# Optimization experiments

Hardware: AMD Instinct MI355X
Metric: run time of the kernel (lower is better)

## Reference

```python
import jax, jax.numpy as jnp
import numpy as np

D, S, E, MPE = 256, 128, 512, 4096
B, N = 2, 4096


def _rope(x):
    # x: (..., n, d); RoPE over axis -2 positions (dim=1 in the torch code)
    n, d = x.shape[-2], x.shape[-1]
    half = d // 2
    pos = jnp.arange(n, dtype=x.dtype)
    inv_freq = 10000.0 ** (-jnp.arange(half, dtype=x.dtype) / half)
    sinusoid = pos[:, None] * inv_freq  # (n, half)
    sin, cos = jnp.sin(sinusoid), jnp.cos(sinusoid)
    x1, x2 = jnp.split(x, 2, axis=-1)
    return jnp.concatenate([x1 * cos - x2 * sin, x2 * cos + x1 * sin], axis=-1)


def setup_inputs() -> dict:
    key = jax.random.key(0)
    ks = jax.random.split(key, 12)
    std = 0.02
    return {
        "query": jax.random.normal(ks[0], (B, N, D), jnp.float32),
        "ln_w": jnp.ones((D,), jnp.float32),
        "ln_b": jnp.zeros((D,), jnp.float32),
        "Wu": jax.random.normal(ks[1], (D, E), jnp.float32) / np.float32(np.sqrt(D)),
        "bu": jnp.zeros((E,), jnp.float32),
        "Wv": jax.random.normal(ks[2], (D, E), jnp.float32) / np.float32(np.sqrt(D)),
        "bv": jnp.zeros((E,), jnp.float32),
        "Wbase": jax.random.normal(ks[3], (D, S), jnp.float32) / np.float32(np.sqrt(D)),
        "bbase": jnp.zeros((S,), jnp.float32),
        "q_w": jax.random.normal(ks[4], (1, S), jnp.float32) * std,
        "q_b": jnp.zeros((1, S), jnp.float32),
        "k_w": jax.random.normal(ks[5], (1, S), jnp.float32) * std,
        "k_b": jnp.zeros((1, S), jnp.float32),
        "w_rel": jax.random.normal(ks[6], (2 * MPE - 1,), jnp.float32) * std,
        "Wo": jax.random.normal(ks[7], (E, D), jnp.float32) / np.float32(np.sqrt(E)),
        "bo": jnp.zeros((D,), jnp.float32),
    }


def reference(query, ln_w, ln_b, Wu, bu, Wv, bv, Wbase, bbase,
              q_w, q_b, k_w, k_b, w_rel, Wo, bo):
    mpe = (w_rel.shape[0] + 1) // 2
    bsz, n, d = query.shape
    # LayerNorm
    mu = query.mean(axis=-1, keepdims=True)
    var = ((query - mu) ** 2).mean(axis=-1, keepdims=True)
    x = (query - mu) * jax.lax.rsqrt(var + 1e-5) * ln_w + ln_b
    # gated projections
    u = jax.nn.silu(x @ Wu + bu)       # (B,N,E)
    v = jax.nn.silu(x @ Wv + bv)       # (B,N,E)
    base = jax.nn.silu(x @ Wbase + bbase)  # (B,N,S)
    q = _rope(base * q_w + q_b)
    k = _rope(base * k_w + k_b)
    qk = jnp.einsum('bms,bns->bmn', q, k)  # (B,N,N)
    # Toeplitz relative-position bias: bias[i,j] = w_rel[mpe-1 + j - i]
    # (equivalent to the torch pad/repeat/reshape construction, sliced to n)
    i = jnp.arange(n)
    bias = w_rel[(mpe - 1) + i[None, :] - i[:, None]]  # (N,N)
    kernel = jnp.square(jax.nn.relu(qk / mpe + bias))
    out = (u * jnp.einsum('bmn,bne->bme', kernel, v)) @ Wo + bo
    return out
```

## Files before the change

kernel.cpp:

```cpp
#include <hip/hip_runtime.h>
#include <hip/hip_bf16.h>
#include <math.h>

typedef __bf16 bf16_8 __attribute__((ext_vector_type(8)));
typedef float f32x4 __attribute__((ext_vector_type(4)));

#define D_ 256
#define S_ 128
#define E_ 512
#define MPE_ 4096
#define B_ 2
#define N_ 4096
#define M_TOT (B_*N_)

__device__ __forceinline__ ushort f2b(float f) {
  union { float f; uint u; } x; x.f = f;
  uint r = (x.u + 0x7FFFu + ((x.u >> 16) & 1u)) >> 16;
  return (ushort)r;
}
__device__ __forceinline__ float b2f(ushort b) {
  union { uint u; float f; } x; x.u = ((uint)b) << 16;
  return x.f;
}

__device__ __forceinline__ void gl_lds16(const void* g, void* l) {
  __builtin_amdgcn_global_load_lds(
      (const __attribute__((address_space(1))) void*)g,
      (__attribute__((address_space(3))) void*)l, 16, 0, 0);
}

__global__ __launch_bounds__(256) void ln_kernel(const float* __restrict__ q,
    const float* __restrict__ w, const float* __restrict__ b,
    ushort* __restrict__ x) {
  int wid = threadIdx.x >> 6, lane = threadIdx.x & 63;
  int row = blockIdx.x * 4 + wid;
  const float* qr = q + (size_t)row * D_;
  float4 v = *(const float4*)(qr + lane * 4);
  float s  = v.x + v.y + v.z + v.w;
  float ss = v.x*v.x + v.y*v.y + v.z*v.z + v.w*v.w;
  #pragma unroll
  for (int off = 32; off; off >>= 1) {
    s  += __shfl_xor(s, off);
    ss += __shfl_xor(ss, off);
  }
  float mu   = s * (1.0f / 256.0f);
  float var  = ss * (1.0f / 256.0f) - mu * mu;
  float rstd = rsqrtf(var + 1e-5f);
  ushort4 o;
  float vv[4] = {v.x, v.y, v.z, v.w};
  ushort ot[4];
  #pragma unroll
  for (int j = 0; j < 4; ++j) {
    int c = lane * 4 + j;
    ot[j] = f2b((vv[j] - mu) * rstd * w[c] + b[c]);
  }
  o.x = ot[0]; o.y = ot[1]; o.z = ot[2]; o.w = ot[3];
  *(ushort4*)(x + (size_t)row * D_ + lane * 4) = o;
}

__global__ void wt_kernel(const float* __restrict__ in, ushort* __restrict__ out,
                          int R, int C) {
  int o = blockIdx.x * 256 + threadIdx.x;
  if (o >= R * C) return;
  int c = o / R, r = o - c * R;
  out[o] = f2b(in[r * C + c]);
}

template<int EPI>
__global__ __launch_bounds__(256) void gemm_kernel(
    const ushort* __restrict__ A, const ushort* __restrict__ Bt,
    const float* __restrict__ bias, void* __restrict__ out,
    int M, int N, int K) {
  __shared__ alignas(16) ushort As[128 * 64];
  __shared__ alignas(16) ushort Bs[64 * 64];
  int tid = threadIdx.x;
  int lane = tid & 63, wid = tid >> 6;
  int m0 = blockIdx.x * 128, n0 = blockIdx.y * 64;
  int r16 = lane & 15, kq = lane >> 4;
  f32x4 acc[2][4] = {};
  for (int k0 = 0; k0 < K; k0 += 64) {
    __syncthreads();
    #pragma unroll
    for (int t = 0; t < 4; ++t) {
      int cid = tid + t * 256;
      int row = cid >> 3, c = cid & 7;
      uint4 d = *(const uint4*)(A + ((size_t)(m0 + row) * K + k0 + c * 8));
      *(uint4*)&As[row * 64 + ((c ^ (row & 7)) * 8)] = d;
    }
    #pragma unroll
    for (int t = 0; t < 2; ++t) {
      int cid = tid + t * 256;
      int row = cid >> 3, c = cid & 7;
      uint4 d = *(const uint4*)(Bt + ((size_t)(n0 + row) * K + k0 + c * 8));
      *(uint4*)&Bs[row * 64 + ((c ^ (row & 7)) * 8)] = d;
    }
    __syncthreads();
    #pragma unroll
    for (int ks = 0; ks < 2; ++ks) {
      bf16_8 af[2], bfr[4];
      int c = ks * 4 + kq;
      #pragma unroll
      for (int fm = 0; fm < 2; ++fm) {
        int r = wid * 32 + fm * 16 + r16;
        af[fm] = *(const bf16_8*)&As[r * 64 + ((c ^ (r & 7)) * 8)];
      }
      #pragma unroll
      for (int fn = 0; fn < 4; ++fn) {
        int r = fn * 16 + r16;
        bfr[fn] = *(const bf16_8*)&Bs[r * 64 + ((c ^ (r & 7)) * 8)];
      }
      #pragma unroll
      for (int fm = 0; fm < 2; ++fm)
        #pragma unroll
        for (int fn = 0; fn < 4; ++fn)
          acc[fm][fn] = __builtin_amdgcn_mfma_f32_16x16x32_bf16(af[fm], bfr[fn], acc[fm][fn], 0, 0, 0);
    }
  }
  #pragma unroll
  for (int fm = 0; fm < 2; ++fm)
    #pragma unroll
    for (int fn = 0; fn < 4; ++fn)
      #pragma unroll
      for (int reg = 0; reg < 4; ++reg) {
        int ml = wid * 32 + fm * 16 + kq * 4 + reg;
        int nl = fn * 16 + r16;
        size_t gm = m0 + ml, gn = n0 + nl;
        float val = acc[fm][fn][reg] + bias[gn];
        if (EPI == 0) {
          float y = val / (1.0f + expf(-val));
          ((ushort*)out)[gm * N + gn] = f2b(y);
        } else if (EPI == 2) {
          float y = val / (1.0f + expf(-val));
          ((ushort*)out)[gn * (size_t)M_TOT + gm] = f2b(y);
        } else {
          ((float*)out)[gm * N + gn] = val;
        }
      }
}

__global__ __launch_bounds__(256) void rope_kernel(const ushort* __restrict__ base,
    const float* __restrict__ qw, const float* __restrict__ qb,
    const float* __restrict__ kw, const float* __restrict__ kb,
    ushort* __restrict__ Q, ushort* __restrict__ Kk) {
  int g = blockIdx.x * 256 + threadIdx.x;
  int row = g >> 6, i = g & 63;
  int n = row & (N_ - 1);
  float invf = powf(10000.0f, -(float)i * (1.0f / 64.0f));
  float sv, cv;
  sincosf((float)n * invf, &sv, &cv);
  const float sc = 0.015625f;
  float b1 = b2f(base[row * S_ + i]), b2 = b2f(base[row * S_ + 64 + i]);
  float x1q = b1 * qw[i] + qb[i], x2q = b2 * qw[64 + i] + qb[64 + i];
  Q[row * S_ + i]      = f2b((x1q * cv - x2q * sv) * sc);
  Q[row * S_ + 64 + i] = f2b((x2q * cv + x1q * sv) * sc);
  float x1k = b1 * kw[i] + kb[i], x2k = b2 * kw[64 + i] + kb[64 + i];
  Kk[row * S_ + i]      = f2b((x1k * cv - x2k * sv) * sc);
  Kk[row * S_ + 64 + i] = f2b((x2k * cv + x1k * sv) * sc);
}

__global__ __launch_bounds__(512, 2) void attn_kernel(
    const ushort* __restrict__ Q, const ushort* __restrict__ Kd,
    const ushort* __restrict__ VT, const ushort* __restrict__ U,
    const float* __restrict__ w_rel, ushort* __restrict__ KVU) {
  __shared__ alignas(16) ushort Ks[2][64 * 128];
  __shared__ alignas(16) ushort Vs[2][128 * 64];
  __shared__ alignas(16) ushort Pb[128 * 64];
  __shared__ alignas(16) float WrLc[2][4][200];
  const int tid = threadIdx.x, lane = tid & 63, wid = tid >> 6;
  const int b = blockIdx.z, m0 = blockIdx.x * 128, e0 = blockIdx.y * 128;
  const int r16 = lane & 15, kq = lane >> 4;
  const int wqm = wid >> 2, wqn = wid & 3;
  const int wpm = wid >> 1, wpe = wid & 1;

  bf16_8 qf[4][4];
  #pragma unroll
  for (int fm = 0; fm < 4; ++fm)
    #pragma unroll
    for (int ks = 0; ks < 4; ++ks)
      qf[fm][ks] = *(const bf16_8*)(Q +
          ((size_t)(b * N_ + m0 + wqm * 64 + fm * 16 + r16) * S_ + ks * 32 + kq * 8));

  auto stage_kv = [&](int bi, int t) {
    int n0s = t * 64;
    #pragma unroll
    for (int tt = 0; tt < 2; ++tt) {
      int p = tt * 512 + tid;
      int row = p >> 4, sc2 = p & 15;
      int cc = sc2 ^ (row & 7);
      gl_lds16(Kd + ((size_t)(b * N_ + n0s + row) * S_ + cc * 8),
               &Ks[bi][(tt * 512 + wid * 64) * 8]);
    }
    #pragma unroll
    for (int tt = 0; tt < 2; ++tt) {
      int p = tt * 512 + tid;
      int er = p >> 3, sc2 = p & 7;
      int nc = sc2 ^ (er & 7);
      gl_lds16(VT + ((size_t)(e0 + er) * M_TOT + b * N_ + n0s + nc * 8),
               &Vs[bi][(tt * 512 + wid * 64) * 8]);
    }
  };

  const int bi0 = tid, bi1 = tid + 512;
  const int bc0 = bi0 / 200, bx0 = bi0 - bc0 * 200;
  const int bc1 = bi1 / 200, bx1 = bi1 - bc1 * 200;
  const bool bp1 = bi1 < 800;
  auto wr_load = [&](int t, float& w0, float& w1) {
    int W0 = 3968 + t * 64 - m0;
    int i0 = W0 + bx0 - 1 - bc0;
    i0 = i0 < 0 ? 0 : (i0 > 8190 ? 8190 : i0);
    w0 = w_rel[i0];
    int i1 = W0 + bx1 - 1 - bc1;
    i1 = i1 < 0 ? 0 : (i1 > 8190 ? 8190 : i1);
    w1 = bp1 ? w_rel[i1] : 0.f;
  };
  auto wr_store = [&](int bi, float w0, float w1) {
    WrLc[bi][bc0][bx0] = w0;
    if (bp1) WrLc[bi][bc1][bx1] = w1;
  };

  f32x4 pv[2][4] = {};

  {
    float w0, w1;
    wr_load(0, w0, w1);
    stage_kv(0, 0);
    wr_store(0, w0, w1);
  }
  asm volatile("s_waitcnt vmcnt(0) lgkmcnt(0)" ::: "memory");
  __builtin_amdgcn_s_barrier();

  const int csel = r16 & 3;
  const int abase = 128 + 4 * kq + 16 * wqn - 64 * wqm - r16 + csel;

  auto body = [&](int CUR, int t) {
    float w0 = 0.f, w1 = 0.f;
    if (t < 63) wr_load(t + 1, w0, w1);
    if (t < 63) stage_kv(CUR ^ 1, t + 1);
    const ushort* ksb = Ks[CUR];
    f32x4 sacc[4] = {};
    __builtin_amdgcn_s_setprio(1);
    #pragma unroll
    for (int ks = 0; ks < 4; ++ks) {
      int r = wqn * 16 + r16;
      int c = ks * 4 + kq;
      bf16_8 kf = *(const bf16_8*)&ksb[r * 128 + ((c ^ (r & 7)) * 8)];
      #pragma unroll
      for (int fm = 0; fm < 4; ++fm)
        sacc[fm] = __builtin_amdgcn_mfma_f32_16x16x32_bf16(kf, qf[fm][ks], sacc[fm], 0, 0, 0);
    }
    __builtin_amdgcn_s_setprio(0);
    if (t < 63) wr_store(CUR ^ 1, w0, w1);
    char* psb = (char*)&Pb[0];
    #pragma unroll
    for (int fm = 0; fm < 4; ++fm) {
      float4 b4 = *(const float4*)&WrLc[CUR][csel][abase - fm * 16];
      float t0 = fmaxf(sacc[fm][0] + b4.x, 0.f);
      float t1 = fmaxf(sacc[fm][1] + b4.y, 0.f);
      float t2 = fmaxf(sacc[fm][2] + b4.z, 0.f);
      float t3 = fmaxf(sacc[fm][3] + b4.w, 0.f);
      t0 *= t0; t1 *= t1; t2 *= t2; t3 *= t3;
      uint p01, p23;
      asm("v_cvt_pk_bf16_f32 %0, %1, %2" : "=v"(p01) : "v"(t0), "v"(t1));
      asm("v_cvt_pk_bf16_f32 %0, %1, %2" : "=v"(p23) : "v"(t2), "v"(t3));
      int mp = wqm * 64 + fm * 16 + r16;
      int nb2 = wqn * 32 + kq * 8;
      uint2 pk; pk.x = p01; pk.y = p23;
      *(uint2*)(psb + ((mp * 128 + nb2) ^ ((mp & 7) << 4))) = pk;
    }
    asm volatile("s_waitcnt lgkmcnt(0)" ::: "memory");
    __builtin_amdgcn_s_barrier();
    const ushort* vsb = Vs[CUR];
    __builtin_amdgcn_s_setprio(1);
    #pragma unroll
    for (int ks = 0; ks < 2; ++ks) {
      bf16_8 pa[2];
      #pragma unroll
      for (int fm = 0; fm < 2; ++fm) {
        int r = wpm * 32 + fm * 16 + r16;
        pa[fm] = *(const bf16_8*)(psb + ((r * 128 + ks * 64 + kq * 16) ^ ((r & 7) << 4)));
      }
      #pragma unroll
      for (int fe = 0; fe < 4; ++fe) {
        int rv = wpe * 64 + fe * 16 + r16;
        int cv = ks * 4 + kq;
        bf16_8 vf = *(const bf16_8*)&vsb[rv * 64 + ((cv ^ (rv & 7)) * 8)];
        #pragma unroll
        for (int fm = 0; fm < 2; ++fm)
          pv[fm][fe] = __builtin_amdgcn_mfma_f32_16x16x32_bf16(pa[fm], vf, pv[fm][fe], 0, 0, 0);
      }
    }
    __builtin_amdgcn_s_setprio(0);
    asm volatile("s_waitcnt vmcnt(0) lgkmcnt(0)" ::: "memory");
    __builtin_amdgcn_s_barrier();
  };

  for (int t2 = 0; t2 < 32; ++t2) {
    body(0, 2 * t2);
    body(1, 2 * t2 + 1);
  }

  #pragma unroll
  for (int fm = 0; fm < 2; ++fm)
    #pragma unroll
    for (int fe = 0; fe < 4; ++fe)
      #pragma unroll
      for (int reg = 0; reg < 4; ++reg) {
        int ml = wpm * 32 + fm * 16 + kq * 4 + reg;
        size_t grow = (size_t)b * N_ + m0 + ml;
        size_t ge = e0 + wpe * 64 + fe * 16 + r16;
        float uu = b2f(U[grow * E_ + ge]);
        KVU[grow * E_ + ge] = f2b(uu * pv[fm][fe][reg]);
      }
}

extern "C" void kernel_launch(void* const* d_in, const int* in_sizes, int n_in,
                              void* d_out, int out_size, void* d_ws, size_t ws_size,
                              hipStream_t stream) {
  const float* query = (const float*)d_in[0];
  const float* ln_w  = (const float*)d_in[1];
  const float* ln_b  = (const float*)d_in[2];
  const float* Wu    = (const float*)d_in[3];
  const float* bu    = (const float*)d_in[4];
  const float* Wv    = (const float*)d_in[5];
  const float* bv    = (const float*)d_in[6];
  const float* Wbase = (const float*)d_in[7];
  const float* bbase = (const float*)d_in[8];
  const float* q_w   = (const float*)d_in[9];
  const float* q_b   = (const float*)d_in[10];
  const float* k_w   = (const float*)d_in[11];
  const float* k_b   = (const float*)d_in[12];
  const float* w_rel = (const float*)d_in[13];
  const float* Wo    = (const float*)d_in[14];
  const float* bo    = (const float*)d_in[15];
  float* out = (float*)d_out;

  char* ws = (char*)d_ws;
  ushort* X    = (ushort*)(ws);
  ushort* U    = (ushort*)(ws + (4u  << 20));
  ushort* VT   = (ushort*)(ws + (12u << 20));
  ushort* BASE = (ushort*)(ws + (20u << 20));
  ushort* Qb   = (ushort*)(ws + (22u << 20));
  ushort* Kb   = (ushort*)(ws + (24u << 20));
  ushort* KVU  = (ushort*)(ws + (26u << 20));
  ushort* WUT  = (ushort*)(ws + (34u << 20));
  ushort* WVT  = (ushort*)(ws + (34u << 20) + 512*256*2);
  ushort* WBT  = (ushort*)(ws + (34u << 20) + 2*512*256*2);
  ushort* WOT  = (ushort*)(ws + (34u << 20) + 2*512*256*2 + 128*256*2);

  ln_kernel<<<2048, 256, 0, stream>>>(query, ln_w, ln_b, X);
  wt_kernel<<<(512*256 + 255) / 256, 256, 0, stream>>>(Wu, WUT, 256, 512);
  wt_kernel<<<(512*256 + 255) / 256, 256, 0, stream>>>(Wv, WVT, 256, 512);
  wt_kernel<<<(128*256 + 255) / 256, 256, 0, stream>>>(Wbase, WBT, 256, 128);
  wt_kernel<<<(512*256 + 255) / 256, 256, 0, stream>>>(Wo, WOT, 512, 256);
  gemm_kernel<0><<<dim3(64, 8), 256, 0, stream>>>(X, WUT, bu, U, 8192, 512, 256);
  gemm_kernel<2><<<dim3(64, 8), 256, 0, stream>>>(X, WVT, bv, VT, 8192, 512, 256);
  gemm_kernel<0><<<dim3(64, 2), 256, 0, stream>>>(X, WBT, bbase, BASE, 8192, 128, 256);
  rope_kernel<<<2048, 256, 0, stream>>>(BASE, q_w, q_b, k_w, k_b, Qb, Kb);
  attn_kernel<<<dim3(32, 4, 2), 512, 0, stream>>>(Qb, Kb, VT, U, w_rel, KVU);
  gemm_kernel<1><<<dim3(64, 4), 256, 0, stream>>>(KVU, WOT, bo, out, 8192, 256, 512);
}
```

Baseline: 159.3 us.

## Software-pipeline PV matmul one tile behind QK and read bias directly from global

Restructures the attention loop so the P·V MFMA for the previous tile runs in the same phase as the QK MFMA for the current tile, using a double-buffered P tile and dropping one barrier per iteration. V staging is split from K staging and issued for the current tile, while the relative-position bias is now loaded straight from global memory per lane instead of being staged through an LDS buffer. The aim is to overlap the two matmul phases and cut synchronisation, at the cost of extra LDS for the second P buffer and many small uncoalesced global bias loads per iteration. Dropping the index clamps means the bias reads depend on the index staying within w_rel's range.

```diff
diff --git a/kernel.cpp b/kernel.cpp
--- a/kernel.cpp
+++ b/kernel.cpp
@@ -164,8 +164,7 @@
     const float* __restrict__ w_rel, ushort* __restrict__ KVU) {
   __shared__ alignas(16) ushort Ks[2][64 * 128];
   __shared__ alignas(16) ushort Vs[2][128 * 64];
-  __shared__ alignas(16) ushort Pb[128 * 64];
-  __shared__ alignas(16) float WrLc[2][4][200];
+  __shared__ alignas(16) ushort Pb[2][128 * 64];
   const int tid = threadIdx.x, lane = tid & 63, wid = tid >> 6;
   const int b = blockIdx.z, m0 = blockIdx.x * 128, e0 = blockIdx.y * 128;
   const int r16 = lane & 15, kq = lane >> 4;
@@ -180,8 +179,8 @@
       qf[fm][ks] = *(const bf16_8*)(Q +
           ((size_t)(b * N_ + m0 + wqm * 64 + fm * 16 + r16) * S_ + ks * 32 + kq * 8));
 
-  auto stage_kv = [&](int bi, int t) {
-    int n0s = t * 64;
+  auto stage_k = [&](int bi, int nt) {
+    int n0s = nt * 64;
     #pragma unroll
     for (int tt = 0; tt < 2; ++tt) {
       int p = tt * 512 + tid;
@@ -190,6 +189,9 @@
       gl_lds16(Kd + ((size_t)(b * N_ + n0s + row) * S_ + cc * 8),
                &Ks[bi][(tt * 512 + wid * 64) * 8]);
     }
+  };
+  auto stage_v = [&](int bi, int nt) {
+    int n0s = nt * 64;
     #pragma unroll
     for (int tt = 0; tt < 2; ++tt) {
       int p = tt * 512 + tid;
@@ -200,42 +202,45 @@
     }
   };
 
-  const int bi0 = tid, bi1 = tid + 512;
-  const int bc0 = bi0 / 200, bx0 = bi0 - bc0 * 200;
-  const int bc1 = bi1 / 200, bx1 = bi1 - bc1 * 200;
-  const bool bp1 = bi1 < 800;
-  auto wr_load = [&](int t, float& w0, float& w1) {
-    int W0 = 3968 + t * 64 - m0;
-    int i0 = W0 + bx0 - 1 - bc0;
-    i0 = i0 < 0 ? 0 : (i0 > 8190 ? 8190 : i0);
-    w0 = w_rel[i0];
-    int i1 = W0 + bx1 - 1 - bc1;
-    i1 = i1 < 0 ? 0 : (i1 > 8190 ? 8190 : i1);
-    w1 = bp1 ? w_rel[i1] : 0.f;
+  f32x4 pv[2][4] = {};
+
+  auto do_pv = [&](const ushort* pr, const ushort* vsb) {
+    __builtin_amdgcn_s_setprio(1);
+    #pragma unroll
+    for (int ks = 0; ks < 2; ++ks) {
+      bf16_8 pa[2];
+      #pragma unroll
+      for (int fm = 0; fm < 2; ++fm) {
+        int r = wpm * 32 + fm * 16 + r16;
+        pa[fm] = *(const bf16_8*)((const char*)pr + ((r * 128 + ks * 64 + kq * 16) ^ ((r & 7) << 4)));
+      }
+      #pragma unroll
+      for (int fe = 0; fe < 4; ++fe) {
+        int rv = wpe * 64 + fe * 16 + r16;
+        int cv = ks * 4 + kq;
+        bf16_8 vf = *(const bf16_8*)&vsb[rv * 64 + ((cv ^ (rv & 7)) * 8)];
+        #pragma unroll
+        for (int fm = 0; fm < 2; ++fm)
+          pv[fm][fe] = __builtin_amdgcn_mfma_f32_16x16x32_bf16(pa[fm], vf, pv[fm][fe], 0, 0, 0);
+      }
+    }
+    __builtin_amdgcn_s_setprio(0);
   };
-  auto wr_store = [&](int bi, float w0, float w1) {
-    WrLc[bi][bc0][bx0] = w0;
-    if (bp1) WrLc[bi][bc1][bx1] = w1;
-  };
-
-  f32x4 pv[2][4] = {};
-
-  {
-    float w0, w1;
-    wr_load(0, w0, w1);
-    stage_kv(0, 0);
-    wr_store(0, w0, w1);
-  }
+
+  stage_k(0, 0);
   asm volatile("s_waitcnt vmcnt(0) lgkmcnt(0)" ::: "memory");
   __builtin_amdgcn_s_barrier();
 
-  const int csel = r16 & 3;
-  const int abase = 128 + 4 * kq + 16 * wqn - 64 * wqm - r16 + csel;
-
   auto body = [&](int CUR, int t) {
-    float w0 = 0.f, w1 = 0.f;
-    if (t < 63) wr_load(t + 1, w0, w1);
-    if (t < 63) stage_kv(CUR ^ 1, t + 1);
+    float bw[4][4];
+    const float* wb = w_rel + (4095 + 64 * t + 16 * wqn + 4 * kq - m0 - 64 * wqm - r16);
+    #pragma unroll
+    for (int fm = 0; fm < 4; ++fm)
+      #pragma unroll
+      for (int rg = 0; rg < 4; ++rg)
+        bw[fm][rg] = wb[rg - 16 * fm];
+    if (t < 63) stage_k(CUR ^ 1, t + 1);
+    stage_v(CUR, t);
     const ushort* ksb = Ks[CUR];
     f32x4 sacc[4] = {};
     __builtin_amdgcn_s_setprio(1);
@@ -249,15 +254,14 @@
         sacc[fm] = __builtin_amdgcn_mfma_f32_16x16x32_bf16(kf, qf[fm][ks], sacc[fm], 0, 0, 0);
     }
     __builtin_amdgcn_s_setprio(0);
-    if (t < 63) wr_store(CUR ^ 1, w0, w1);
-    char* psb = (char*)&Pb[0];
+    if (t > 0) do_pv((const ushort*)&Pb[CUR ^ 1][0], &Vs[CUR ^ 1][0]);
+    char* psb = (char*)&Pb[CUR][0];
     #pragma unroll
     for (int fm = 0; fm < 4; ++fm) {
-      float4 b4 = *(const float4*)&WrLc[CUR][csel][abase - fm * 16];
-      float t0 = fmaxf(sacc[fm][0] + b4.x, 0.f);
-      float t1 = fmaxf(sacc[fm][1] + b4.y, 0.f);
-      float t2 = fmaxf(sacc[fm][2] + b4.z, 0.f);
-      float t3 = fmaxf(sacc[fm][3] + b4.w, 0.f);
+      float t0 = fmaxf(sacc[fm][0] + bw[fm][0], 0.f);
+      float t1 = fmaxf(sacc[fm][1] + bw[fm][1], 0.f);
+      float t2 = fmaxf(sacc[fm][2] + bw[fm][2], 0.f);
+      float t3 = fmaxf(sacc[fm][3] + bw[fm][3], 0.f);
       t0 *= t0; t1 *= t1; t2 *= t2; t3 *= t3;
       uint p01, p23;
       asm("v_cvt_pk_bf16_f32 %0, %1, %2" : "=v"(p01) : "v"(t0), "v"(t1));
@@ -267,29 +271,6 @@
       uint2 pk; pk.x = p01; pk.y = p23;
       *(uint2*)(psb + ((mp * 128 + nb2) ^ ((mp & 7) << 4))) = pk;
     }
-    asm volatile("s_waitcnt lgkmcnt(0)" ::: "memory");
-    __builtin_amdgcn_s_barrier();
-    const ushort* vsb = Vs[CUR];
-    __builtin_amdgcn_s_setprio(1);
-    #pragma unroll
-    for (int ks = 0; ks < 2; ++ks) {
-      bf16_8 pa[2];
-      #pragma unroll
-      for (int fm = 0; fm < 2; ++fm) {
-        int r = wpm * 32 + fm * 16 + r16;
-        pa[fm] = *(const bf16_8*)(psb + ((r * 128 + ks * 64 + kq * 16) ^ ((r & 7) << 4)));
-      }
-      #pragma unroll
-      for (int fe = 0; fe < 4; ++fe) {
-        int rv = wpe * 64 + fe * 16 + r16;
-        int cv = ks * 4 + kq;
-        bf16_8 vf = *(const bf16_8*)&vsb[rv * 64 + ((cv ^ (rv & 7)) * 8)];
-        #pragma unroll
-        for (int fm = 0; fm < 2; ++fm)
-          pv[fm][fe] = __builtin_amdgcn_mfma_f32_16x16x32_bf16(pa[fm], vf, pv[fm][fe], 0, 0, 0);
-      }
-    }
-    __builtin_amdgcn_s_setprio(0);
     asm volatile("s_waitcnt vmcnt(0) lgkmcnt(0)" ::: "memory");
     __builtin_amdgcn_s_barrier();
   };
@@ -298,6 +279,7 @@
     body(0, 2 * t2);
     body(1, 2 * t2 + 1);
   }
+  do_pv((const ushort*)&Pb[1][0], &Vs[1][0]);
 
   #pragma unroll
   for (int fm = 0; fm < 2; ++fm)
```

Measured after the change: 146.1 us. 1.09x faster.
